# Kernel tuning notes

Measured on AMD Instinct MI355X. Metric: run time of the kernel, lower is better.

## Reference

```python
import jax, jax.numpy as jnp
import numpy as np

N, IN_DIM, HID = 8192, 256, 128


def _glorot(key, shape):
    lim = float(np.sqrt(6.0 / (shape[0] + shape[1])))
    return jax.random.uniform(key, shape, jnp.float32, -lim, lim)


def setup_inputs() -> dict:
    key = jax.random.key(0)
    ks = jax.random.split(key, 16)
    return {
        "x": jax.random.normal(ks[0], (N, IN_DIM), jnp.float32),
        "XY_Adj": jnp.zeros((N, N), jnp.float32),  # unused: overwritten by Cos_Adj in forward
        "w0": _glorot(ks[1], (IN_DIM, HID)),
        "w1": _glorot(ks[2], (IN_DIM, HID)),
        "Wq1": _glorot(ks[3], (IN_DIM, HID)), "bq1": jnp.zeros((HID,), jnp.float32),
        "Wk1": _glorot(ks[4], (IN_DIM, HID)), "bk1": jnp.zeros((HID,), jnp.float32),
        "Wv1": _glorot(ks[5], (IN_DIM, HID)), "bv1": jnp.zeros((HID,), jnp.float32),
        "Ws1": _glorot(ks[6], (IN_DIM, HID)), "bs1": jnp.zeros((HID,), jnp.float32),
        "Wq4": _glorot(ks[7], (HID, IN_DIM)), "bq4": jnp.zeros((IN_DIM,), jnp.float32),
        "Wk4": _glorot(ks[8], (HID, IN_DIM)), "bk4": jnp.zeros((IN_DIM,), jnp.float32),
        "Wv4": _glorot(ks[9], (HID, IN_DIM)), "bv4": jnp.zeros((IN_DIM,), jnp.float32),
        "Ws4": _glorot(ks[10], (HID, IN_DIM)), "bs4": jnp.zeros((IN_DIM,), jnp.float32),
    }


def _cos_adj(x, w0, w1):
    # Dense cosine-similarity adjacency, as in Cos_Adj.forward
    theta = x @ w0  # [N, HID]
    phi = x @ w1    # [N, HID]
    tn = jnp.linalg.norm(theta, axis=1, keepdims=True)  # [N,1]
    pn = jnp.linalg.norm(phi, axis=1, keepdims=True)    # [N,1]
    return (theta @ phi.T) / (tn @ pn.T + 1e-20)        # [N,N]


def _tconv(h, Wq, bq, Wk, bk, Wv, bv, Ws, bs):
    # PyG TransformerConv (heads=1, root_weight=True) on the fully-connected
    # graph produced by coo_matrix(sim_graph) == dense all-pairs attention.
    q = h @ Wq + bq
    k = h @ Wk + bk
    v = h @ Wv + bv
    scale = 1.0 / np.sqrt(q.shape[-1])
    attn = jax.nn.softmax((q @ k.T) * scale, axis=-1)  # [N,N]
    return attn @ v + (h @ Ws + bs)


def reference(x, XY_Adj, w0, w1,
              Wq1, bq1, Wk1, bk1, Wv1, bv1, Ws1, bs1,
              Wq4, bq4, Wk4, bk4, Wv4, bv4, Ws4, bs4):
    # Adjacency values only define the edge set (all N^2 pairs nonzero for
    # generic inputs); TransformerConv recomputes attention coefficients.
    sim = _cos_adj(x, w0, w1)  # noqa: F841 (edge set = nonzeros = all pairs)
    h1 = jax.nn.elu(_tconv(x, Wq1, bq1, Wk1, bk1, Wv1, bv1, Ws1, bs1))
    out = _tconv(h1, Wq4, bq4, Wk4, bk4, Wv4, bv4, Ws4, bs4)
    return out
```

## Files before the change

kernel.cpp:

```cpp
#include <hip/hip_runtime.h>

#define N_ROWS 8192
#define IN_DIM 256
#define HID 128

typedef __attribute__((ext_vector_type(8))) short bf16x8;
typedef __attribute__((ext_vector_type(4))) float f32x4;

__device__ __forceinline__ unsigned short f2bf(float f) {
    union { float f; unsigned u; } v; v.f = f;
    unsigned r = (v.u + 0x7FFFu + ((v.u >> 16) & 1u)) >> 16;
    return (unsigned short)r;
}

__device__ __forceinline__ unsigned cvt_pk_bf16(float lo, float hi) {
    unsigned r;
    asm("v_cvt_pk_bf16_f32 %0, %1, %2" : "=v"(r) : "v"(lo), "v"(hi));
    return r;
}

__global__ void pack_weights(const float* __restrict__ W0, const float* __restrict__ W1,
                             const float* __restrict__ W2, const float* __restrict__ W3,
                             const float* __restrict__ b0, const float* __restrict__ b1,
                             const float* __restrict__ b2, const float* __restrict__ b3,
                             unsigned short* __restrict__ WT, float* __restrict__ B,
                             int K, int HO)
{
    int NT = 4 * HO;
    int idx = blockIdx.x * blockDim.x + threadIdx.x;
    if (idx < NT * K) {
        int n = idx / K, k = idx - n * K;
        int s = n / HO, sn = n - s * HO;
        const float* W = (s == 0) ? W0 : (s == 1) ? W1 : (s == 2) ? W2 : W3;
        WT[idx] = f2bf(W[k * HO + sn]);
    }
    if (idx < NT) {
        int s = idx / HO, sn = idx - s * HO;
        const float* b = (s == 0) ? b0 : (s == 1) ? b1 : (s == 2) ? b2 : b3;
        B[idx] = b[sn];
    }
}

__global__ void cast_x(const float* __restrict__ in, unsigned short* __restrict__ out, int n) {
    int i = blockIdx.x * blockDim.x + threadIdx.x;
    if (i < n) out[i] = f2bf(in[i]);
}

__global__ void transpose_bf16(const unsigned short* __restrict__ in,
                               unsigned short* __restrict__ out, int R, int C)
{
    __shared__ unsigned short t[32][33];
    const int tx = threadIdx.x, ty = threadIdx.y;
    const int r0 = blockIdx.y * 32, c0 = blockIdx.x * 32;
    #pragma unroll
    for (int j = 0; j < 32; j += 8)
        t[ty + j][tx] = in[(size_t)(r0 + ty + j) * C + c0 + tx];
    __syncthreads();
    #pragma unroll
    for (int j = 0; j < 32; j += 8)
        out[(size_t)(c0 + ty + j) * R + r0 + tx] = t[tx][ty + j];
}

template<int K>
__global__ __launch_bounds__(256) void proj_gemm(
    const unsigned short* __restrict__ A, const unsigned short* __restrict__ WT,
    const float* __restrict__ bias,
    unsigned short* __restrict__ qo, unsigned short* __restrict__ ko,
    unsigned short* __restrict__ vo, float* __restrict__ skip,
    int NT, float qScale)
{
    const int lane = threadIdx.x & 63;
    const int wid = (blockIdx.x * blockDim.x + threadIdx.x) >> 6;
    const int nStrips = NT / 64;
    const int mTile = wid / nStrips;
    const int nBase = (wid - mTile * nStrips) * 64;
    const int l15 = lane & 15, lg = lane >> 4;
    const int HO = NT >> 2;

    f32x4 acc[4];
    #pragma unroll
    for (int c = 0; c < 4; ++c) acc[c] = f32x4{0.f, 0.f, 0.f, 0.f};

    const unsigned short* Ap = A + (size_t)(mTile * 16 + l15) * K + lg * 8;
    #pragma unroll
    for (int t = 0; t < K / 32; ++t) {
        bf16x8 a = *(const bf16x8*)(Ap + t * 32);
        #pragma unroll
        for (int c = 0; c < 4; ++c) {
            bf16x8 b = *(const bf16x8*)(WT + (size_t)(nBase + c * 16 + l15) * K + t * 32 + lg * 8);
            acc[c] = __builtin_amdgcn_mfma_f32_16x16x32_bf16(a, b, acc[c], 0, 0, 0);
        }
    }
    #pragma unroll
    for (int c = 0; c < 4; ++c) {
        int col = nBase + c * 16 + l15;
        int sec = col / HO, sc = col - sec * HO;
        float bv = bias[col];
        #pragma unroll
        for (int r = 0; r < 4; ++r) {
            int mrow = mTile * 16 + lg * 4 + r;
            float val = acc[c][r] + bv;
            size_t o = (size_t)mrow * HO + sc;
            if (sec == 0) qo[o] = f2bf(val * qScale);
            else if (sec == 1) ko[o] = f2bf(val);
            else if (sec == 2) vo[o] = f2bf(val);
            else skip[o] = val;
        }
    }
}

template<int D, int KB, int Q2>
__global__ __launch_bounds__(512) void attn_partial(
    const unsigned short* __restrict__ Qm,
    const unsigned short* __restrict__ Km,
    const unsigned short* __restrict__ VTg,
    float* __restrict__ accOut, float* __restrict__ mOut, float* __restrict__ lOut,
    int chunkLen)
{
    constexpr int TPB = 512;
    constexpr int LK = D + 8;
    constexpr int LV = KB + 8;
    constexpr int DT = D / 16;
    constexpr int CT = KB / 16;
    constexpr int KS = KB / 32;
    constexpr int QW = 16 * Q2;
    static_assert(KB * D / 8 / TPB == 2, "two K staging int4s per thread");
    static_assert(D * KB / 8 / TPB == 2, "two V staging int4s per thread");
    __shared__ __align__(16) unsigned short Kl[KB * LK];
    __shared__ __align__(16) unsigned short VTl[D * LV];

    const int tid = threadIdx.x;
    const int lane = tid & 63;
    const int w = tid >> 6;
    const int l15 = lane & 15, lg = lane >> 4;
    const int qrow = blockIdx.x * (8 * QW) + w * QW;
    const int kStart = blockIdx.y * chunkLen;
    const size_t NN = N_ROWS;

    const int kr0 = tid / (D / 8), kc0 = tid - kr0 * (D / 8);
    const int kr1 = (tid + TPB) / (D / 8), kc1 = (tid + TPB) - kr1 * (D / 8);
    const int kg0 = kr0 * D + kc0 * 8, kl0 = kr0 * LK + kc0 * 8;
    const int kg1 = kr1 * D + kc1 * 8, kl1 = kr1 * LK + kc1 * 8;
    const int vr0 = tid / (KB / 8), vc0 = tid - vr0 * (KB / 8);
    const int vr1 = (tid + TPB) / (KB / 8), vc1 = (tid + TPB) - vr1 * (KB / 8);
    const int vg0 = vr0 * (int)NN + vc0 * 8, vl0 = vr0 * LV + vc0 * 8;
    const int vg1 = vr1 * (int)NN + vc1 * 8, vl1 = vr1 * LV + vc1 * 8;

    bf16x8 qf[Q2][D / 32];
    #pragma unroll
    for (int m = 0; m < Q2; ++m)
        #pragma unroll
        for (int t = 0; t < D / 32; ++t)
            qf[m][t] = *(const bf16x8*)(Qm + (size_t)(qrow + m * 16 + l15) * D + t * 32 + lg * 8);

    f32x4 acc[Q2][DT];
    float mReg[Q2], lReg[Q2];
    #pragma unroll
    for (int m = 0; m < Q2; ++m) {
        #pragma unroll
        for (int dt = 0; dt < DT; ++dt) acc[m][dt] = f32x4{0.f, 0.f, 0.f, 0.f};
        mReg[m] = -__builtin_inff();
        lReg[m] = 0.f;
    }

    const int nt = chunkLen / KB;
    const unsigned short* Kp = Km + (size_t)kStart * D;
    const unsigned short* Vp = VTg + kStart;
    int4 pk0 = *(const int4*)(Kp + kg0);
    int4 pk1 = *(const int4*)(Kp + kg1);
    int4 pv0 = *(const int4*)(Vp + vg0);
    int4 pv1 = *(const int4*)(Vp + vg1);

    for (int t = 0; t < nt; ++t) {
        __syncthreads();
        *(int4*)(&Kl[kl0]) = pk0;
        *(int4*)(&Kl[kl1]) = pk1;
        *(int4*)(&VTl[vl0]) = pv0;
        *(int4*)(&VTl[vl1]) = pv1;
        __syncthreads();
        if (t + 1 < nt) {
            const unsigned short* KpN = Kp + (size_t)(t + 1) * KB * D;
            const unsigned short* VpN = Vp + (t + 1) * KB;
            pk0 = *(const int4*)(KpN + kg0);
            pk1 = *(const int4*)(KpN + kg1);
            pv0 = *(const int4*)(VpN + vg0);
            pv1 = *(const int4*)(VpN + vg1);
        }
        f32x4 sT[Q2][CT];
        __builtin_amdgcn_s_setprio(1);
        #pragma unroll
        for (int c = 0; c < CT; ++c) {
            #pragma unroll
            for (int m = 0; m < Q2; ++m) sT[m][c] = f32x4{0.f, 0.f, 0.f, 0.f};
            #pragma unroll
            for (int tt = 0; tt < D / 32; ++tt) {
                bf16x8 kf = *(const bf16x8*)(&Kl[(c * 16 + l15) * LK + tt * 32 + lg * 8]);
                #pragma unroll
                for (int m = 0; m < Q2; ++m)
                    sT[m][c] = __builtin_amdgcn_mfma_f32_16x16x32_bf16(kf, qf[m][tt], sT[m][c], 0, 0, 0);
            }
        }
        __builtin_amdgcn_s_setprio(0);
        float pmax[Q2];
        bool need = false;
        #pragma unroll
        for (int m = 0; m < Q2; ++m) {
            float v = sT[m][0][0];
            #pragma unroll
            for (int c = 0; c < CT; ++c)
                #pragma unroll
                for (int r = 0; r < 4; ++r) v = fmaxf(v, sT[m][c][r]);
            pmax[m] = v;
            need = need || (v > mReg[m] + 8.f);
        }
        if (__any(need)) {
            #pragma unroll
            for (int m = 0; m < Q2; ++m) {
                float v = pmax[m];
                v = fmaxf(v, __shfl_xor(v, 16));
                v = fmaxf(v, __shfl_xor(v, 32));
                float mN = fmaxf(mReg[m], v);
                float al = exp2f(mReg[m] - mN);
                mReg[m] = mN;
                lReg[m] *= al;
                #pragma unroll
                for (int dt = 0; dt < DT; ++dt) acc[m][dt] *= al;
            }
        }
        unsigned Wp[Q2][CT][2];
        #pragma unroll
        for (int m = 0; m < Q2; ++m) {
            float lsum = 0.f;
            #pragma unroll
            for (int c = 0; c < CT; ++c) {
                float p0 = exp2f(sT[m][c][0] - mReg[m]);
                float p1 = exp2f(sT[m][c][1] - mReg[m]);
                float p2 = exp2f(sT[m][c][2] - mReg[m]);
                float p3 = exp2f(sT[m][c][3] - mReg[m]);
                lsum += (p0 + p1) + (p2 + p3);
                Wp[m][c][0] = cvt_pk_bf16(p0, p1);
                Wp[m][c][1] = cvt_pk_bf16(p2, p3);
            }
            lReg[m] += lsum;
        }
        #pragma unroll
        for (int ks = 0; ks < KS; ++ks) {
            bf16x8 pbv[Q2];
            #pragma unroll
            for (int m = 0; m < Q2; ++m) {
                unsigned x0 = Wp[m][2 * ks][0], x1 = Wp[m][2 * ks][1];
                unsigned x2 = Wp[m][2 * ks + 1][0], x3 = Wp[m][2 * ks + 1][1];
                const bool g1 = (lg & 2) != 0, g0 = (lg & 1) != 0;
                unsigned s0 = g1 ? x0 : x2, s1 = g1 ? x1 : x3;
                unsigned r0 = __shfl_xor(s0, 32), r1 = __shfl_xor(s1, 32);
                unsigned k0 = g1 ? x2 : x0, k1 = g1 ? x3 : x1;
                unsigned t0 = (g0 != g1) ? k0 : r0, t1 = (g0 != g1) ? k1 : r1;
                unsigned q0 = __shfl_xor(t0, 16), q1 = __shfl_xor(t1, 16);
                union { unsigned u[4]; bf16x8 v; } pb;
                pb.u[0] = g0 ? q0 : (g1 ? r0 : k0);
                pb.u[1] = g0 ? q1 : (g1 ? r1 : k1);
                pb.u[2] = g0 ? (g1 ? k0 : r0) : q0;
                pb.u[3] = g0 ? (g1 ? k1 : r1) : q1;
                pbv[m] = pb.v;
            }
            __builtin_amdgcn_s_setprio(1);
            #pragma unroll
            for (int dt = 0; dt < DT; ++dt) {
                bf16x8 va = *(const bf16x8*)(&VTl[(dt * 16 + l15) * LV + ks * 32 + lg * 8]);
                #pragma unroll
                for (int m = 0; m < Q2; ++m)
                    acc[m][dt] = __builtin_amdgcn_mfma_f32_16x16x32_bf16(va, pbv[m], acc[m][dt], 0, 0, 0);
            }
            __builtin_amdgcn_s_setprio(0);
        }
    }

    #pragma unroll
    for (int m = 0; m < Q2; ++m) {
        float lv = lReg[m];
        lv += __shfl_xor(lv, 16);
        lv += __shfl_xor(lv, 32);
        float* accRow = accOut + ((size_t)blockIdx.y * NN + qrow + m * 16 + l15) * D + lg * 4;
        #pragma unroll
        for (int dt = 0; dt < DT; ++dt)
            *(f32x4*)(accRow + dt * 16) = acc[m][dt];
        if (lg == 0) {
            mOut[blockIdx.y * NN + qrow + m * 16 + l15] = mReg[m];
            lOut[blockIdx.y * NN + qrow + m * 16 + l15] = lv;
        }
    }
}

template<int D, bool ELU>
__global__ void combine_kernel(const float* __restrict__ acc, const float* __restrict__ mArr,
                               const float* __restrict__ lArr, const float* __restrict__ skip,
                               float* __restrict__ outF, unsigned short* __restrict__ outB,
                               int CH)
{
    const int row = blockIdx.x;
    const int d = threadIdx.x;
    const size_t NN = N_ROWS;
    float mStar = -__builtin_inff();
    for (int c = 0; c < CH; ++c) mStar = fmaxf(mStar, mArr[c * NN + row]);
    float denom = 0.f, val = 0.f;
    for (int c = 0; c < CH; ++c) {
        float wgt = exp2f(mArr[c * NN + row] - mStar);
        denom += wgt * lArr[c * NN + row];
        val += wgt * acc[((size_t)c * NN + row) * D + d];
    }
    float v = val / denom + skip[(size_t)row * D + d];
    if (ELU) {
        v = (v > 0.f) ? v : expm1f(v);
        outB[(size_t)row * D + d] = f2bf(v);
    } else {
        outF[(size_t)row * D + d] = v;
    }
}

extern "C" void kernel_launch(void* const* d_in, const int* in_sizes, int n_in,
                              void* d_out, int out_size, void* d_ws, size_t ws_size,
                              hipStream_t stream)
{
    (void)in_sizes; (void)n_in; (void)out_size;
    const float* x   = (const float*)d_in[0];
    const float* Wq1 = (const float*)d_in[4];
    const float* bq1 = (const float*)d_in[5];
    const float* Wk1 = (const float*)d_in[6];
    const float* bk1 = (const float*)d_in[7];
    const float* Wv1 = (const float*)d_in[8];
    const float* bv1 = (const float*)d_in[9];
    const float* Ws1 = (const float*)d_in[10];
    const float* bs1 = (const float*)d_in[11];
    const float* Wq4 = (const float*)d_in[12];
    const float* bq4 = (const float*)d_in[13];
    const float* Wk4 = (const float*)d_in[14];
    const float* bk4 = (const float*)d_in[15];
    const float* Wv4 = (const float*)d_in[16];
    const float* bv4 = (const float*)d_in[17];
    const float* Ws4 = (const float*)d_in[18];
    const float* bs4 = (const float*)d_in[19];
    float* out = (float*)d_out;

    const int N = N_ROWS;
    size_t off = 0;
    auto alloc = [&](size_t bytes) -> void* {
        void* p = (char*)d_ws + off;
        off = (off + bytes + 255) & ~(size_t)255;
        return p;
    };
    unsigned short* xb  = (unsigned short*)alloc((size_t)N * IN_DIM * 2);
    unsigned short* WT1 = (unsigned short*)alloc((size_t)512 * 256 * 2);
    float* B1           = (float*)alloc(512 * 4);
    unsigned short* WT4 = (unsigned short*)alloc((size_t)1024 * 128 * 2);
    float* B4           = (float*)alloc(1024 * 4);
    unsigned short* q1  = (unsigned short*)alloc((size_t)N * HID * 2);
    unsigned short* k1  = (unsigned short*)alloc((size_t)N * HID * 2);
    unsigned short* v1  = (unsigned short*)alloc((size_t)N * HID * 2);
    unsigned short* VT1g= (unsigned short*)alloc((size_t)HID * N * 2);
    float* skip1        = (float*)alloc((size_t)N * HID * 4);
    unsigned short* h1  = (unsigned short*)alloc((size_t)N * HID * 2);
    unsigned short* q4  = (unsigned short*)alloc((size_t)N * IN_DIM * 2);
    unsigned short* k4  = (unsigned short*)alloc((size_t)N * IN_DIM * 2);
    unsigned short* v4  = (unsigned short*)alloc((size_t)N * IN_DIM * 2);
    unsigned short* VT4g= (unsigned short*)alloc((size_t)IN_DIM * N * 2);
    float* skip4        = (float*)alloc((size_t)N * IN_DIM * 4);

    size_t fixedEnd = off;
    size_t perCH = (size_t)N * 4 * 4 + (size_t)N * HID * 4 + (size_t)N * IN_DIM * 4 + 4096;
    int CH = 8;
    while (CH > 1 && fixedEnd + (size_t)CH * perCH > ws_size) CH >>= 1;

    float* m1   = (float*)alloc((size_t)CH * N * 4);
    float* l1   = (float*)alloc((size_t)CH * N * 4);
    float* m2   = (float*)alloc((size_t)CH * N * 4);
    float* l2   = (float*)alloc((size_t)CH * N * 4);
    float* acc1 = (float*)alloc((size_t)CH * N * HID * 4);
    float* acc2 = (float*)alloc((size_t)CH * N * IN_DIM * 4);
    if (off > ws_size && CH == 1) acc2 = out;

    const float LOG2E = 1.4426950408889634f;
    const float qs1 = 0.088388347648318447f * LOG2E;
    const float qs2 = 0.0625f * LOG2E;

    pack_weights<<<dim3((512 * 256 + 255) / 256), dim3(256), 0, stream>>>(
        Wq1, Wk1, Wv1, Ws1, bq1, bk1, bv1, bs1, WT1, B1, 256, 128);
    pack_weights<<<dim3((1024 * 128 + 255) / 256), dim3(256), 0, stream>>>(
        Wq4, Wk4, Wv4, Ws4, bq4, bk4, bv4, bs4, WT4, B4, 128, 256);
    cast_x<<<dim3((N * IN_DIM + 255) / 256), dim3(256), 0, stream>>>(x, xb, N * IN_DIM);

    proj_gemm<256><<<dim3((N / 16) * (512 / 64) / 4), dim3(256), 0, stream>>>(
        xb, WT1, B1, q1, k1, v1, skip1, 512, qs1);
    transpose_bf16<<<dim3(HID / 32, N / 32), dim3(32, 8), 0, stream>>>(v1, VT1g, N, HID);
    attn_partial<128, 64, 2><<<dim3(N / 256, CH), dim3(512), 0, stream>>>(
        q1, k1, VT1g, acc1, m1, l1, N / CH);
    combine_kernel<128, true><<<dim3(N), dim3(128), 0, stream>>>(
        acc1, m1, l1, skip1, (float*)nullptr, h1, CH);

    proj_gemm<128><<<dim3((N / 16) * (1024 / 64) / 4), dim3(256), 0, stream>>>(
        h1, WT4, B4, q4, k4, v4, skip4, 1024, qs2);
    transpose_bf16<<<dim3(IN_DIM / 32, N / 32), dim3(32, 8), 0, stream>>>(v4, VT4g, N, IN_DIM);
    attn_partial<256, 32, 2><<<dim3(N / 256, CH), dim3(512), 0, stream>>>(
        q4, k4, VT4g, acc2, m2, l2, N / CH);
    combine_kernel<256, false><<<dim3(N), dim3(256), 0, stream>>>(
        acc2, m2, l2, skip4, out, (unsigned short*)nullptr, CH);
}
```

Before: 271.0 us.

## Generalize attention tiling and split second-layer V dimension across grid z

The attention kernel is templated on separate key and value widths, block size and staging counts. It now uses 4-wave blocks with 64 query rows per wave and 32-key tiles. The second layer splits its 256-wide value output into two 128-wide halves along grid z, so each block keeps a smaller accumulator and the grid has twice as many blocks. The cost is that Q·Kᵀ scores and softmax statistics for layer 2 are computed twice, once per half, and both halves write identical m/l values.

```diff
diff --git a/kernel.cpp b/kernel.cpp
--- a/kernel.cpp
+++ b/kernel.cpp
@@ -109,82 +109,92 @@
     }
 }
 
-template<int D, int KB, int Q2>
-__global__ __launch_bounds__(512) void attn_partial(
+template<int DK, int DV, int DF, int KB, int Q2, int TPB>
+__global__ __launch_bounds__(TPB) void attn_partial(
     const unsigned short* __restrict__ Qm,
     const unsigned short* __restrict__ Km,
     const unsigned short* __restrict__ VTg,
     float* __restrict__ accOut, float* __restrict__ mOut, float* __restrict__ lOut,
     int chunkLen)
 {
-    constexpr int TPB = 512;
-    constexpr int LK = D + 8;
+    constexpr int LK = DK + 8;
     constexpr int LV = KB + 8;
-    constexpr int DT = D / 16;
+    constexpr int DTV = DV / 16;
     constexpr int CT = KB / 16;
     constexpr int KS = KB / 32;
     constexpr int QW = 16 * Q2;
-    static_assert(KB * D / 8 / TPB == 2, "two K staging int4s per thread");
-    static_assert(D * KB / 8 / TPB == 2, "two V staging int4s per thread");
+    constexpr int WAVES = TPB / 64;
+    constexpr int PKI = KB * DK / 8 / TPB;
+    constexpr int PVI = DV * KB / 8 / TPB;
+    static_assert(KB * DK / 8 % TPB == 0 && DV * KB / 8 % TPB == 0, "staging divisibility");
     __shared__ __align__(16) unsigned short Kl[KB * LK];
-    __shared__ __align__(16) unsigned short VTl[D * LV];
+    __shared__ __align__(16) unsigned short VTl[DV * LV];
 
     const int tid = threadIdx.x;
     const int lane = tid & 63;
     const int w = tid >> 6;
     const int l15 = lane & 15, lg = lane >> 4;
-    const int qrow = blockIdx.x * (8 * QW) + w * QW;
+    const int qrow = blockIdx.x * (WAVES * QW) + w * QW;
     const int kStart = blockIdx.y * chunkLen;
+    const int vOff = blockIdx.z * DV;
     const size_t NN = N_ROWS;
 
-    const int kr0 = tid / (D / 8), kc0 = tid - kr0 * (D / 8);
-    const int kr1 = (tid + TPB) / (D / 8), kc1 = (tid + TPB) - kr1 * (D / 8);
-    const int kg0 = kr0 * D + kc0 * 8, kl0 = kr0 * LK + kc0 * 8;
-    const int kg1 = kr1 * D + kc1 * 8, kl1 = kr1 * LK + kc1 * 8;
-    const int vr0 = tid / (KB / 8), vc0 = tid - vr0 * (KB / 8);
-    const int vr1 = (tid + TPB) / (KB / 8), vc1 = (tid + TPB) - vr1 * (KB / 8);
-    const int vg0 = vr0 * (int)NN + vc0 * 8, vl0 = vr0 * LV + vc0 * 8;
-    const int vg1 = vr1 * (int)NN + vc1 * 8, vl1 = vr1 * LV + vc1 * 8;
-
-    bf16x8 qf[Q2][D / 32];
+    int kgo[PKI], klo[PKI], vgo[PVI], vlo[PVI];
+    #pragma unroll
+    for (int i = 0; i < PKI; ++i) {
+        int idx = tid + i * TPB;
+        int r = idx / (DK / 8), c = idx - r * (DK / 8);
+        kgo[i] = r * DK + c * 8;
+        klo[i] = r * LK + c * 8;
+    }
+    #pragma unroll
+    for (int i = 0; i < PVI; ++i) {
+        int idx = tid + i * TPB;
+        int r = idx / (KB / 8), c = idx - r * (KB / 8);
+        vgo[i] = r * (int)NN + c * 8;
+        vlo[i] = r * LV + c * 8;
+    }
+
+    bf16x8 qf[Q2][DK / 32];
     #pragma unroll
     for (int m = 0; m < Q2; ++m)
         #pragma unroll
-        for (int t = 0; t < D / 32; ++t)
-            qf[m][t] = *(const bf16x8*)(Qm + (size_t)(qrow + m * 16 + l15) * D + t * 32 + lg * 8);
-
-    f32x4 acc[Q2][DT];
+        for (int t = 0; t < DK / 32; ++t)
+            qf[m][t] = *(const bf16x8*)(Qm + (size_t)(qrow + m * 16 + l15) * DK + t * 32 + lg * 8);
+
+    f32x4 acc[Q2][DTV];
     float mReg[Q2], lReg[Q2];
     #pragma unroll
     for (int m = 0; m < Q2; ++m) {
         #pragma unroll
-        for (int dt = 0; dt < DT; ++dt) acc[m][dt] = f32x4{0.f, 0.f, 0.f, 0.f};
+        for (int dt = 0; dt < DTV; ++dt) acc[m][dt] = f32x4{0.f, 0.f, 0.f, 0.f};
         mReg[m] = -__builtin_inff();
         lReg[m] = 0.f;
     }
 
     const int nt = chunkLen / KB;
-    const unsigned short* Kp = Km + (size_t)kStart * D;
-    const unsigned short* Vp = VTg + kStart;
-    int4 pk0 = *(const int4*)(Kp + kg0);
-    int4 pk1 = *(const int4*)(Kp + kg1);
-    int4 pv0 = *(const int4*)(Vp + vg0);
-    int4 pv1 = *(const int4*)(Vp + vg1);
+    const unsigned short* Kp = Km + (size_t)kStart * DK;
+    const unsigned short* Vp = VTg + (size_t)vOff * NN + kStart;
+    int4 pk[PKI], pv[PVI];
+    #pragma unroll
+    for (int i = 0; i < PKI; ++i) pk[i] = *(const int4*)(Kp + kgo[i]);
+    #pragma unroll
+    for (int i = 0; i < PVI; ++i) pv[i] = *(const int4*)(Vp + vgo[i]);
 
     for (int t = 0; t < nt; ++t) {
         __syncthreads();
-        *(int4*)(&Kl[kl0]) = pk0;
-        *(int4*)(&Kl[kl1]) = pk1;
-        *(int4*)(&VTl[vl0]) = pv0;
-        *(int4*)(&VTl[vl1]) = pv1;
+        #pragma unroll
+        for (int i = 0; i < PKI; ++i) *(int4*)(&Kl[klo[i]]) = pk[i];
+        #pragma unroll
+        for (int i = 0; i < PVI; ++i) *(int4*)(&VTl[vlo[i]]) = pv[i];
         __syncthreads();
         if (t + 1 < nt) {
-            const unsigned short* KpN = Kp + (size_t)(t + 1) * KB * D;
+            const unsigned short* KpN = Kp + (size_t)(t + 1) * KB * DK;
             const unsigned short* VpN = Vp + (t + 1) * KB;
-            pk0 = *(const int4*)(KpN + kg0);
-            pk1 = *(const int4*)(KpN + kg1);
-            pv0 = *(const int4*)(VpN + vg0);
-            pv1 = *(const int4*)(VpN + vg1);
+            #pragma unroll
+            for (int i = 0; i < PKI; ++i) pk[i] = *(const int4*)(KpN + kgo[i]);
+            #pragma unroll
+            for (int i = 0; i < PVI; ++i) pv[i] = *(const int4*)(VpN + vgo[i]);
         }
         f32x4 sT[Q2][CT];
         __builtin_amdgcn_s_setprio(1);
@@ -193,7 +203,7 @@
             #pragma unroll
             for (int m = 0; m < Q2; ++m) sT[m][c] = f32x4{0.f, 0.f, 0.f, 0.f};
             #pragma unroll
-            for (int tt = 0; tt < D / 32; ++tt) {
+            for (int tt = 0; tt < DK / 32; ++tt) {
                 bf16x8 kf = *(const bf16x8*)(&Kl[(c * 16 + l15) * LK + tt * 32 + lg * 8]);
                 #pragma unroll
                 for (int m = 0; m < Q2; ++m)
@@ -224,7 +234,7 @@
                 mReg[m] = mN;
                 lReg[m] *= al;
                 #pragma unroll
-                for (int dt = 0; dt < DT; ++dt) acc[m][dt] *= al;
+                for (int dt = 0; dt < DTV; ++dt) acc[m][dt] *= al;
             }
         }
         unsigned Wp[Q2][CT][2];
@@ -265,7 +275,7 @@
             }
             __builtin_amdgcn_s_setprio(1);
             #pragma unroll
-            for (int dt = 0; dt < DT; ++dt) {
+            for (int dt = 0; dt < DTV; ++dt) {
                 bf16x8 va = *(const bf16x8*)(&VTl[(dt * 16 + l15) * LV + ks * 32 + lg * 8]);
                 #pragma unroll
                 for (int m = 0; m < Q2; ++m)
@@ -280,9 +290,9 @@
         float lv = lReg[m];
         lv += __shfl_xor(lv, 16);
         lv += __shfl_xor(lv, 32);
-        float* accRow = accOut + ((size_t)blockIdx.y * NN + qrow + m * 16 + l15) * D + lg * 4;
-        #pragma unroll
-        for (int dt = 0; dt < DT; ++dt)
+        float* accRow = accOut + ((size_t)blockIdx.y * NN + qrow + m * 16 + l15) * DF + vOff + lg * 4;
+        #pragma unroll
+        for (int dt = 0; dt < DTV; ++dt)
             *(f32x4*)(accRow + dt * 16) = acc[m][dt];
         if (lg == 0) {
             mOut[blockIdx.y * NN + qrow + m * 16 + l15] = mReg[m];
@@ -391,7 +401,7 @@
     proj_gemm<256><<<dim3((N / 16) * (512 / 64) / 4), dim3(256), 0, stream>>>(
         xb, WT1, B1, q1, k1, v1, skip1, 512, qs1);
     transpose_bf16<<<dim3(HID / 32, N / 32), dim3(32, 8), 0, stream>>>(v1, VT1g, N, HID);
-    attn_partial<128, 64, 2><<<dim3(N / 256, CH), dim3(512), 0, stream>>>(
+    attn_partial<128, 128, 128, 32, 4, 256><<<dim3(N / 256, CH, 1), dim3(256), 0, stream>>>(
         q1, k1, VT1g, acc1, m1, l1, N / CH);
     combine_kernel<128, true><<<dim3(N), dim3(128), 0, stream>>>(
         acc1, m1, l1, skip1, (float*)nullptr, h1, CH);
@@ -399,7 +409,7 @@
     proj_gemm<128><<<dim3((N / 16) * (1024 / 64) / 4), dim3(256), 0, stream>>>(
         h1, WT4, B4, q4, k4, v4, skip4, 1024, qs2);
     transpose_bf16<<<dim3(IN_DIM / 32, N / 32), dim3(32, 8), 0, stream>>>(v4, VT4g, N, IN_DIM);
-    attn_partial<256, 32, 2><<<dim3(N / 256, CH), dim3(512), 0, stream>>>(
+    attn_partial<256, 128, 256, 32, 4, 256><<<dim3(N / 256, CH, 2), dim3(256), 0, stream>>>(
         q4, k4, VT4g, acc2, m2, l2, N / CH);
     combine_kernel<256, false><<<dim3(N), dim3(256), 0, stream>>>(
         acc2, m2, l2, skip4, out, (unsigned short*)nullptr, CH);
```

Result: slower. 527.8 us (+94.7%).

## Double-buffer K/V tiles in attention and write V transposed from projection

Applied to the files above, without the earlier changes.

The attention kernel now keeps two LDS buffers for K and V^T tiles. The next tile is stored into the alternate buffer after the current tile's compute, so each iteration needs one barrier instead of two. Separately, the projection GEMM writes V straight into transposed layout, which removes the two transpose kernel launches and their intermediate buffers. In exchange, LDS use doubles, which may lower occupancy, and the transposed V stores from the GEMM epilogue are strided, uncoalesced 2-byte writes.

```diff
diff --git a/kernel.cpp b/kernel.cpp
--- a/kernel.cpp
+++ b/kernel.cpp
@@ -46,27 +46,12 @@
     if (i < n) out[i] = f2bf(in[i]);
 }
 
-__global__ void transpose_bf16(const unsigned short* __restrict__ in,
-                               unsigned short* __restrict__ out, int R, int C)
-{
-    __shared__ unsigned short t[32][33];
-    const int tx = threadIdx.x, ty = threadIdx.y;
-    const int r0 = blockIdx.y * 32, c0 = blockIdx.x * 32;
-    #pragma unroll
-    for (int j = 0; j < 32; j += 8)
-        t[ty + j][tx] = in[(size_t)(r0 + ty + j) * C + c0 + tx];
-    __syncthreads();
-    #pragma unroll
-    for (int j = 0; j < 32; j += 8)
-        out[(size_t)(c0 + ty + j) * R + r0 + tx] = t[tx][ty + j];
-}
-
 template<int K>
 __global__ __launch_bounds__(256) void proj_gemm(
     const unsigned short* __restrict__ A, const unsigned short* __restrict__ WT,
     const float* __restrict__ bias,
     unsigned short* __restrict__ qo, unsigned short* __restrict__ ko,
-    unsigned short* __restrict__ vo, float* __restrict__ skip,
+    unsigned short* __restrict__ vt, float* __restrict__ skip,
     int NT, float qScale)
 {
     const int lane = threadIdx.x & 63;
@@ -100,11 +85,10 @@
         for (int r = 0; r < 4; ++r) {
             int mrow = mTile * 16 + lg * 4 + r;
             float val = acc[c][r] + bv;
-            size_t o = (size_t)mrow * HO + sc;
-            if (sec == 0) qo[o] = f2bf(val * qScale);
-            else if (sec == 1) ko[o] = f2bf(val);
-            else if (sec == 2) vo[o] = f2bf(val);
-            else skip[o] = val;
+            if (sec == 0) qo[(size_t)mrow * HO + sc] = f2bf(val * qScale);
+            else if (sec == 1) ko[(size_t)mrow * HO + sc] = f2bf(val);
+            else if (sec == 2) vt[(size_t)sc * N_ROWS + mrow] = f2bf(val);
+            else skip[(size_t)mrow * HO + sc] = val;
         }
     }
 }
@@ -126,8 +110,8 @@
     constexpr int QW = 16 * Q2;
     static_assert(KB * D / 8 / TPB == 2, "two K staging int4s per thread");
     static_assert(D * KB / 8 / TPB == 2, "two V staging int4s per thread");
-    __shared__ __align__(16) unsigned short Kl[KB * LK];
-    __shared__ __align__(16) unsigned short VTl[D * LV];
+    __shared__ __align__(16) unsigned short Kl[2][KB * LK];
+    __shared__ __align__(16) unsigned short VTl[2][D * LV];
 
     const int tid = threadIdx.x;
     const int lane = tid & 63;
@@ -166,19 +150,20 @@
     const int nt = chunkLen / KB;
     const unsigned short* Kp = Km + (size_t)kStart * D;
     const unsigned short* Vp = VTg + kStart;
+
     int4 pk0 = *(const int4*)(Kp + kg0);
     int4 pk1 = *(const int4*)(Kp + kg1);
     int4 pv0 = *(const int4*)(Vp + vg0);
     int4 pv1 = *(const int4*)(Vp + vg1);
+    *(int4*)(&Kl[0][kl0]) = pk0;
+    *(int4*)(&Kl[0][kl1]) = pk1;
+    *(int4*)(&VTl[0][vl0]) = pv0;
+    *(int4*)(&VTl[0][vl1]) = pv1;
+    int cur = 0;
 
     for (int t = 0; t < nt; ++t) {
-        __syncthreads();
-        *(int4*)(&Kl[kl0]) = pk0;
-        *(int4*)(&Kl[kl1]) = pk1;
-        *(int4*)(&VTl[vl0]) = pv0;
-        *(int4*)(&VTl[vl1]) = pv1;
-        __syncthreads();
-        if (t + 1 < nt) {
+        const bool more = (t + 1 < nt);
+        if (more) {
             const unsigned short* KpN = Kp + (size_t)(t + 1) * KB * D;
             const unsigned short* VpN = Vp + (t + 1) * KB;
             pk0 = *(const int4*)(KpN + kg0);
@@ -186,6 +171,9 @@
             pv0 = *(const int4*)(VpN + vg0);
             pv1 = *(const int4*)(VpN + vg1);
         }
+        __syncthreads();
+        const unsigned short* Kc = &Kl[cur][0];
+        const unsigned short* Vc = &VTl[cur][0];
         f32x4 sT[Q2][CT];
         __builtin_amdgcn_s_setprio(1);
         #pragma unroll
@@ -194,7 +182,7 @@
             for (int m = 0; m < Q2; ++m) sT[m][c] = f32x4{0.f, 0.f, 0.f, 0.f};
             #pragma unroll
             for (int tt = 0; tt < D / 32; ++tt) {
-                bf16x8 kf = *(const bf16x8*)(&Kl[(c * 16 + l15) * LK + tt * 32 + lg * 8]);
+                bf16x8 kf = *(const bf16x8*)(&Kc[(c * 16 + l15) * LK + tt * 32 + lg * 8]);
                 #pragma unroll
                 for (int m = 0; m < Q2; ++m)
                     sT[m][c] = __builtin_amdgcn_mfma_f32_16x16x32_bf16(kf, qf[m][tt], sT[m][c], 0, 0, 0);
@@ -266,13 +254,20 @@
             __builtin_amdgcn_s_setprio(1);
             #pragma unroll
             for (int dt = 0; dt < DT; ++dt) {
-                bf16x8 va = *(const bf16x8*)(&VTl[(dt * 16 + l15) * LV + ks * 32 + lg * 8]);
+                bf16x8 va = *(const bf16x8*)(&Vc[(dt * 16 + l15) * LV + ks * 32 + lg * 8]);
                 #pragma unroll
                 for (int m = 0; m < Q2; ++m)
                     acc[m][dt] = __builtin_amdgcn_mfma_f32_16x16x32_bf16(va, pbv[m], acc[m][dt], 0, 0, 0);
             }
             __builtin_amdgcn_s_setprio(0);
         }
+        if (more) {
+            *(int4*)(&Kl[cur ^ 1][kl0]) = pk0;
+            *(int4*)(&Kl[cur ^ 1][kl1]) = pk1;
+            *(int4*)(&VTl[cur ^ 1][vl0]) = pv0;
+            *(int4*)(&VTl[cur ^ 1][vl1]) = pv1;
+        }
+        cur ^= 1;
     }
 
     #pragma unroll
@@ -355,13 +350,11 @@
     float* B4           = (float*)alloc(1024 * 4);
     unsigned short* q1  = (unsigned short*)alloc((size_t)N * HID * 2);
     unsigned short* k1  = (unsigned short*)alloc((size_t)N * HID * 2);
-    unsigned short* v1  = (unsigned short*)alloc((size_t)N * HID * 2);
     unsigned short* VT1g= (unsigned short*)alloc((size_t)HID * N * 2);
     float* skip1        = (float*)alloc((size_t)N * HID * 4);
     unsigned short* h1  = (unsigned short*)alloc((size_t)N * HID * 2);
     unsigned short* q4  = (unsigned short*)alloc((size_t)N * IN_DIM * 2);
     unsigned short* k4  = (unsigned short*)alloc((size_t)N * IN_DIM * 2);
-    unsigned short* v4  = (unsigned short*)alloc((size_t)N * IN_DIM * 2);
     unsigned short* VT4g= (unsigned short*)alloc((size_t)IN_DIM * N * 2);
     float* skip4        = (float*)alloc((size_t)N * IN_DIM * 4);
 
@@ -389,16 +382,14 @@
     cast_x<<<dim3((N * IN_DIM + 255) / 256), dim3(256), 0, stream>>>(x, xb, N * IN_DIM);
 
     proj_gemm<256><<<dim3((N / 16) * (512 / 64) / 4), dim3(256), 0, stream>>>(
-        xb, WT1, B1, q1, k1, v1, skip1, 512, qs1);
-    transpose_bf16<<<dim3(HID / 32, N / 32), dim3(32, 8), 0, stream>>>(v1, VT1g, N, HID);
+        xb, WT1, B1, q1, k1, VT1g, skip1, 512, qs1);
     attn_partial<128, 64, 2><<<dim3(N / 256, CH), dim3(512), 0, stream>>>(
         q1, k1, VT1g, acc1, m1, l1, N / CH);
     combine_kernel<128, true><<<dim3(N), dim3(128), 0, stream>>>(
         acc1, m1, l1, skip1, (float*)nullptr, h1, CH);
 
     proj_gemm<128><<<dim3((N / 16) * (1024 / 64) / 4), dim3(256), 0, stream>>>(
-        h1, WT4, B4, q4, k4, v4, skip4, 1024, qs2);
-    transpose_bf16<<<dim3(IN_DIM / 32, N / 32), dim3(32, 8), 0, stream>>>(v4, VT4g, N, IN_DIM);
+        h1, WT4, B4, q4, k4, VT4g, skip4, 1024, qs2);
     attn_partial<256, 32, 2><<<dim3(N / 256, CH), dim3(512), 0, stream>>>(
         q4, k4, VT4g, acc2, m2, l2, N / CH);
     combine_kernel<256, false><<<dim3(N), dim3(256), 0, stream>>>(
```

Result: slower. 286.9 us (+5.8%).
